# Kernel tuning notes

Measured on AMD Instinct MI355X. Metric: run time of the kernel, lower is better.

## Reference

```python
import jax, jax.numpy as jnp
import numpy as np
from jax.scipy.linalg import expm

B, S, D = 8, 2048, 1024          # batch, seq, input_dim
C, CD = 16, 64                   # num_concepts, concept_dim
L = C * CD                       # latent_dim = 1024
ALPHA, BETA = 0.3, 1.0
LN_EPS = 1e-5                    # torch nn.LayerNorm default


def layer_norm(x, g, b):
    m = jnp.mean(x, axis=-1, keepdims=True)
    v = jnp.mean(jnp.square(x - m), axis=-1, keepdims=True)
    return (x - m) * jax.lax.rsqrt(v + LN_EPS) * g + b


def setup_inputs() -> dict:
    key = jax.random.key(0)
    ks = jax.random.split(key, 8)
    sc = 0.02
    return {
        "x": jax.random.normal(ks[0], (B, S, D), jnp.float32),
        # encoder: Linear(D, 2L) + LayerNorm(2L)
        "enc_w": jax.random.normal(ks[1], (2 * L, D), jnp.float32) * sc,
        "enc_b": jnp.zeros((2 * L,), jnp.float32),
        "enc_g": jnp.ones((2 * L,), jnp.float32),
        "enc_bt": jnp.zeros((2 * L,), jnp.float32),
        # DAG weights [C, C] (torch inits zeros; use small random for non-trivial math)
        "dag_w": jax.random.normal(ks[2], (C, C), jnp.float32) * 0.1,
        # per-concept transforms: Linear(CD,CD) -> LN(CD) -> ReLU -> Linear(CD,CD), stacked over C
        "cw1": jax.random.normal(ks[3], (C, CD, CD), jnp.float32) * sc,
        "cb1": jnp.zeros((C, CD), jnp.float32),
        "cg": jnp.ones((C, CD), jnp.float32),
        "cbt": jnp.zeros((C, CD), jnp.float32),
        "cw2": jax.random.normal(ks[4], (C, CD, CD), jnp.float32) * sc,
        "cb2": jnp.zeros((C, CD), jnp.float32),
        # decoder: Linear(L,L) -> LN(L) -> ReLU -> Linear(L,D)
        "dec_w1": jax.random.normal(ks[5], (L, L), jnp.float32) * sc,
        "dec_b1": jnp.zeros((L,), jnp.float32),
        "dec_g": jnp.ones((L,), jnp.float32),
        "dec_bt": jnp.zeros((L,), jnp.float32),
        "dec_w2": jax.random.normal(ks[6], (D, L), jnp.float32) * sc,
        "dec_b2": jnp.zeros((D,), jnp.float32),
    }


def reference(x, enc_w, enc_b, enc_g, enc_bt, dag_w, cw1, cb1, cg, cbt, cw2, cb2,
              dec_w1, dec_b1, dec_g, dec_bt, dec_w2, dec_b2):
    # ---- encode ----
    h = layer_norm(jnp.einsum('bsd,kd->bsk', x, enc_w) + enc_b, enc_g, enc_bt)  # [B,S,2L]
    mu, logvar = jnp.split(h, 2, axis=-1)                                        # [B,S,L] each
    z = mu  # eval-mode reparameterize

    # ---- causal transform ----
    zc = z.reshape(B, S, C, CD)                                   # [B,S,C,CD]
    dag = jnp.tril(jax.nn.softplus(dag_w), k=-1)                  # [C,C]
    z_causal = zc + jnp.einsum('ij,bsjd->bsid', dag, zc)          # [B,S,C,CD]

    # per-concept Linear -> LN -> ReLU -> Linear, batched over concept axis
    t = jnp.einsum('bsce,cde->bscd', z_causal, cw1) + cb1         # [B,S,C,CD]
    t = layer_norm(t, cg, cbt)
    t = jax.nn.relu(t)
    t = jnp.einsum('bsce,cde->bscd', t, cw2) + cb2
    z_t = t.reshape(B, S, L)

    # ---- decode ----
    d = layer_norm(jnp.einsum('bsl,kl->bsk', z_t, dec_w1) + dec_b1, dec_g, dec_bt)
    d = jax.nn.relu(d)
    x_recon = jnp.einsum('bsl,dl->bsd', d, dec_w2) + dec_b2        # [B,S,D]

    # ---- losses ----
    recon_loss = jnp.mean(jnp.square(x_recon - x))
    kl_loss = -0.5 * jnp.mean(1.0 + logvar - jnp.square(mu) - jnp.exp(logvar))
    dag_loss = jnp.sum(jnp.abs(dag)) + jnp.trace(expm(dag))
    total_loss = recon_loss + ALPHA * kl_loss + BETA * dag_loss
    return x_recon, total_loss, kl_loss, recon_loss, dag_loss
```

## Files before the change

### kernel.cpp

```cpp
#include <hip/hip_runtime.h>
#include <stdint.h>


#define NTOK   16384
#define DIM    1024
#define NC     16
#define CD     64
#define NOUT_ELEMS 16777216

typedef float f32x4 __attribute__((ext_vector_type(4)));
typedef __bf16 bf16x8 __attribute__((ext_vector_type(8)));
typedef unsigned short u16x4 __attribute__((ext_vector_type(4)));
typedef unsigned short u16x8 __attribute__((ext_vector_type(8)));

__device__ float g_scal[3];
__device__ float g_part[512];

__device__ __forceinline__ float b2f(uint16_t u) {
  union { uint32_t i; float f; } v; v.i = ((uint32_t)u) << 16; return v.f;
}
__device__ __forceinline__ uint16_t f2b(float f) {
  union { float f; uint32_t i; } v; v.f = f;
  uint32_t x = v.i;
  return (uint16_t)((x + 0x7fffu + ((x >> 16) & 1u)) >> 16);
}

__device__ __forceinline__ void gload_lds16(const uint16_t* g, uint16_t* l) {
  __builtin_amdgcn_global_load_lds(
      (const __attribute__((address_space(1))) void*)g,
      (__attribute__((address_space(3))) void*)l, 16, 0, 0);
}

__device__ __forceinline__ void cvt8(const float* s, uint16_t* d) {
  const f32x4 a = *(const f32x4*)s;
  const f32x4 b = *(const f32x4*)(s + 4);
  u16x8 o;
  o[0]=f2b(a[0]); o[1]=f2b(a[1]); o[2]=f2b(a[2]); o[3]=f2b(a[3]);
  o[4]=f2b(b[0]); o[5]=f2b(b[1]); o[6]=f2b(b[2]); o[7]=f2b(b[3]);
  *(u16x8*)d = o;
}

__global__ __launch_bounds__(256) void cvt_x_kernel(
    const float* __restrict__ src, uint16_t* __restrict__ dst)
{
  const int i = blockIdx.x * 256 + threadIdx.x;
  cvt8(src + (size_t)i * 8, dst + (size_t)i * 8);
}

__global__ __launch_bounds__(256) void cvt_weights_kernel(
    const float* __restrict__ ew, const float* __restrict__ d1,
    const float* __restrict__ d2, const float* __restrict__ c1,
    const float* __restrict__ c2, uint16_t* __restrict__ out)
{
  const int i = blockIdx.x * 256 + threadIdx.x;
  const float* src; uint16_t* dst; int off;
  if (i < 262144)      { src = ew; dst = out;           off = i; }
  else if (i < 393216) { src = d1; dst = out + 2097152; off = i - 262144; }
  else if (i < 524288) { src = d2; dst = out + 3145728; off = i - 393216; }
  else if (i < 532480) { src = c1; dst = out + 4194304; off = i - 524288; }
  else                 { src = c2; dst = out + 4259840; off = i - 532480; }
  cvt8(src + (size_t)off * 8, dst + (size_t)off * 8);
}

template<int BM, int BN, int WM, int WN, typename TC, bool SPLIT>
__global__ __launch_bounds__(256) void gemm_bt_kernel(
    const uint16_t* __restrict__ A, const uint16_t* __restrict__ Wm,
    const float* __restrict__ bias, TC* __restrict__ C0, TC* __restrict__ C1,
    int K, int lda, int ldw, int ldc,
    int csA, int csW, int csB, int csC)
{
  constexpr int BK = 64;
  static_assert(WM * WN == 4, "4 waves");
  constexpr int MI = BM / (WM * 16);
  constexpr int NI = BN / (WN * 16);
  constexpr int AI = (BM * BK * 2) / 4096;
  constexpr int WI = (BN * BK * 2) / 4096;
  static_assert((BM * BK * 2) % 4096 == 0 && (BN * BK * 2) % 4096 == 0, "");

  __shared__ __align__(16) uint16_t lds[BM * BK + BN * BK];
  uint16_t* As = lds;
  uint16_t* Ws = lds + BM * BK;

  const int cz = blockIdx.z;
  A    += (size_t)cz * csA;
  Wm   += (size_t)cz * csW;
  bias += cz * csB;

  const int tid  = threadIdx.x;
  const int wave = tid >> 6;
  const int lane = tid & 63;
  const int q    = lane >> 4;
  const int r16  = lane & 15;
  const int wm   = wave / WN;
  const int wn   = wave % WN;

  const int bm = blockIdx.x * BM;
  const int bn = blockIdx.y * BN;

  const int sr = tid >> 3;
  const int pc = tid & 7;

  f32x4 acc[MI][NI] = {};

  for (int k0 = 0; k0 < K; k0 += BK) {
#pragma unroll
    for (int i = 0; i < AI; ++i) {
      const int r = i * 32 + sr;
      const int c = pc ^ (r & 7);
      const uint16_t* g = A + (size_t)(bm + r) * lda + k0 + c * 8;
      gload_lds16(g, (uint16_t*)((char*)As + i * 4096 + wave * 1024));
    }
#pragma unroll
    for (int i = 0; i < WI; ++i) {
      const int r = i * 32 + sr;
      const int c = pc ^ (r & 7);
      const uint16_t* g = Wm + (size_t)(bn + r) * ldw + k0 + c * 8;
      gload_lds16(g, (uint16_t*)((char*)Ws + i * 4096 + wave * 1024));
    }
    __syncthreads();

#pragma unroll
    for (int ks = 0; ks < 2; ++ks) {
      bf16x8 af[MI], wf[NI];
#pragma unroll
      for (int mi = 0; mi < MI; ++mi) {
        const int row = wm * (MI * 16) + mi * 16 + r16;
        const int c   = (ks * 4 + q) ^ (row & 7);
        af[mi] = *(const bf16x8*)(As + row * BK + c * 8);
      }
#pragma unroll
      for (int ni = 0; ni < NI; ++ni) {
        const int col = wn * (NI * 16) + ni * 16 + r16;
        const int c   = (ks * 4 + q) ^ (col & 7);
        wf[ni] = *(const bf16x8*)(Ws + col * BK + c * 8);
      }
#pragma unroll
      for (int mi = 0; mi < MI; ++mi)
#pragma unroll
        for (int ni = 0; ni < NI; ++ni)
          acc[mi][ni] = __builtin_amdgcn_mfma_f32_16x16x32_bf16(
              af[mi], wf[ni], acc[mi][ni], 0, 0, 0);
    }
    __syncthreads();
  }

  TC* Cq = C0;
  int cb = bn;
  if constexpr (SPLIT) {
    if (bn >= 1024) { Cq = C1; cb = bn - 1024; }
  }
  Cq += (size_t)cz * csC;
#pragma unroll
  for (int ni = 0; ni < NI; ++ni) {
    const int loc = wn * (NI * 16) + ni * 16 + r16;
    const float bv = bias[bn + loc];
#pragma unroll
    for (int mi = 0; mi < MI; ++mi) {
      const int rbase = bm + wm * (MI * 16) + mi * 16 + q * 4;
#pragma unroll
      for (int r = 0; r < 4; ++r) {
        const float v = acc[mi][ni][r] + bv;
        if constexpr (sizeof(TC) == 2)
          Cq[(size_t)(rbase + r) * ldc + cb + loc] = f2b(v);
        else
          Cq[(size_t)(rbase + r) * ldc + cb + loc] = v;
      }
    }
  }
}

__global__ __launch_bounds__(256) void kl_causal_kernel(
    const uint16_t* __restrict__ lv, uint16_t* __restrict__ mu,
    const float* __restrict__ g, const float* __restrict__ b,
    const float* __restrict__ dag_w)
{
  __shared__ __align__(16) float zsh[1024];
  __shared__ float dg[256];
  __shared__ float red[8];
  __shared__ float red2[4];
  const int tid = threadIdx.x;
  const int tok = blockIdx.x;
  const int e0  = tid * 4;

  {
    const int di = tid >> 4, dj = tid & 15;
    dg[tid] = (dj < di) ? log1pf(expf(dag_w[tid])) : 0.f;
  }

  const uint16_t* lvp = lv + (size_t)tok * 1024;
  uint16_t*       mup = mu + (size_t)tok * 1024;

  const u16x4 m4 = *(const u16x4*)(mup + e0);
  const u16x4 l4 = *(const u16x4*)(lvp + e0);
  float xm[4], xl[4];
  float s1 = 0.f, s2 = 0.f;
#pragma unroll
  for (int k = 0; k < 4; ++k) {
    xm[k] = b2f(m4[k]);
    xl[k] = b2f(l4[k]);
    s1 += xm[k] + xl[k];
    s2 += xm[k] * xm[k] + xl[k] * xl[k];
  }
#pragma unroll
  for (int m = 1; m < 64; m <<= 1) {
    s1 += __shfl_xor(s1, m);
    s2 += __shfl_xor(s2, m);
  }
  const int wave = tid >> 6, lane = tid & 63;
  if (lane == 0) { red[wave] = s1; red[4 + wave] = s2; }
  __syncthreads();
  s1 = red[0] + red[1] + red[2] + red[3];
  s2 = red[4] + red[5] + red[6] + red[7];
  const float mean = s1 * (1.f / 2048.f);
  const float var  = s2 * (1.f / 2048.f) - mean * mean;
  const float rs   = rsqrtf(var + 1e-5f);

  const f32x4 g4m = *(const f32x4*)(g + e0);
  const f32x4 b4m = *(const f32x4*)(b + e0);
  const f32x4 g4l = *(const f32x4*)(g + 1024 + e0);
  const f32x4 b4l = *(const f32x4*)(b + 1024 + e0);
  float kl = 0.f;
  f32x4 z;
#pragma unroll
  for (int k = 0; k < 4; ++k) {
    z[k] = (xm[k] - mean) * rs * g4m[k] + b4m[k];
    const float y = (xl[k] - mean) * rs * g4l[k] + b4l[k];
    kl += 1.f + y - z[k] * z[k] - expf(y);
  }
  *(f32x4*)(zsh + e0) = z;
#pragma unroll
  for (int m = 1; m < 64; m <<= 1) kl += __shfl_xor(kl, m);
  if (lane == 0) red2[wave] = kl;
  __syncthreads();
  if (tid == 0)
    atomicAdd(&g_part[tok & 255], red2[0] + red2[1] + red2[2] + red2[3]);

  const int i  = e0 >> 6;
  const int d0 = e0 & 63;
  f32x4 s = *(const f32x4*)(zsh + e0);
  for (int j = 0; j < i; ++j) {
    const float w = dg[i * 16 + j];
    const f32x4 zj = *(const f32x4*)(zsh + j * 64 + d0);
    s[0] += w * zj[0]; s[1] += w * zj[1]; s[2] += w * zj[2]; s[3] += w * zj[3];
  }
  u16x4 o;
#pragma unroll
  for (int k = 0; k < 4; ++k) o[k] = f2b(s[k]);
  *(u16x4*)(mup + e0) = o;
}

__global__ __launch_bounds__(256) void ln_relu_kernel(
    uint16_t* __restrict__ data, const float* __restrict__ g,
    const float* __restrict__ b)
{
  const int tid = threadIdx.x;
  const int e0  = tid * 4;
  uint16_t* p = data + (size_t)blockIdx.x * 1024;

  const u16x4 v4 = *(const u16x4*)(p + e0);
  float x[4];
  float s1 = 0.f, s2 = 0.f;
#pragma unroll
  for (int k = 0; k < 4; ++k) {
    x[k] = b2f(v4[k]);
    s1 += x[k];
    s2 += x[k] * x[k];
  }
#pragma unroll
  for (int m = 1; m < 64; m <<= 1) {
    s1 += __shfl_xor(s1, m);
    s2 += __shfl_xor(s2, m);
  }
  __shared__ float red[8];
  const int wave = tid >> 6, lane = tid & 63;
  if (lane == 0) { red[wave] = s1; red[4 + wave] = s2; }
  __syncthreads();
  s1 = red[0] + red[1] + red[2] + red[3];
  s2 = red[4] + red[5] + red[6] + red[7];
  const float mean = s1 * (1.f / 1024.f);
  const float var  = s2 * (1.f / 1024.f) - mean * mean;
  const float rs   = rsqrtf(var + 1e-5f);

  const f32x4 g4 = *(const f32x4*)(g + e0);
  const f32x4 b4 = *(const f32x4*)(b + e0);
  u16x4 o;
#pragma unroll
  for (int k = 0; k < 4; ++k) {
    const float y = (x[k] - mean) * rs * g4[k] + b4[k];
    o[k] = f2b(fmaxf(y, 0.f));
  }
  *(u16x4*)(p + e0) = o;
}

__global__ __launch_bounds__(256) void ln_cd_kernel(
    uint16_t* __restrict__ t, const float* __restrict__ cg,
    const float* __restrict__ cbt)
{
  const int tid = threadIdx.x;
  const int sub = tid >> 4;
  const int le  = tid & 15;
  const int gidx = blockIdx.x * 16 + sub;
  const int c = gidx & 15;
  const size_t off = (size_t)gidx * 64 + le * 4;

  const u16x4 v4 = *(const u16x4*)(t + off);
  float x[4];
  float s1 = 0.f, s2 = 0.f;
#pragma unroll
  for (int k = 0; k < 4; ++k) {
    x[k] = b2f(v4[k]);
    s1 += x[k];
    s2 += x[k] * x[k];
  }
#pragma unroll
  for (int m = 1; m < 16; m <<= 1) {
    s1 += __shfl_xor(s1, m);
    s2 += __shfl_xor(s2, m);
  }
  const float mean = s1 * (1.f / 64.f);
  const float var  = s2 * (1.f / 64.f) - mean * mean;
  const float rs   = rsqrtf(var + 1e-5f);

  const f32x4 cg4  = *(const f32x4*)(cg + c * 64 + le * 4);
  const f32x4 cbt4 = *(const f32x4*)(cbt + c * 64 + le * 4);
  u16x4 o;
#pragma unroll
  for (int k = 0; k < 4; ++k) {
    const float y = (x[k] - mean) * rs * cg4[k] + cbt4[k];
    o[k] = f2b(fmaxf(y, 0.f));
  }
  *(u16x4*)(t + off) = o;
}

__global__ __launch_bounds__(256) void recon_kernel(
    const float* __restrict__ xr, const float* __restrict__ x, int n4)
{
  const f32x4* xr4 = (const f32x4*)xr;
  const f32x4* x4  = (const f32x4*)x;
  float s = 0.f;
  for (int i = blockIdx.x * 256 + threadIdx.x; i < n4; i += gridDim.x * 256) {
    const f32x4 d = xr4[i] - x4[i];
    s += d[0] * d[0] + d[1] * d[1] + d[2] * d[2] + d[3] * d[3];
  }
#pragma unroll
  for (int m = 1; m < 64; m <<= 1) s += __shfl_xor(s, m);
  __shared__ float red[4];
  const int wave = threadIdx.x >> 6, lane = threadIdx.x & 63;
  if (lane == 0) red[wave] = s;
  __syncthreads();
  if (threadIdx.x == 0)
    atomicAdd(&g_part[256 + (blockIdx.x & 255)], red[0] + red[1] + red[2] + red[3]);
}

__global__ __launch_bounds__(256) void dag_init_kernel(
    const float* __restrict__ dag_w)
{
  const int t = threadIdx.x;
  g_part[t] = 0.f;
  g_part[256 + t] = 0.f;
  const int i = t >> 4, j = t & 15;
  const float v = (j < i) ? log1pf(expf(dag_w[t])) : 0.f;
  float s = v;
#pragma unroll
  for (int m = 1; m < 64; m <<= 1) s += __shfl_xor(s, m);
  __shared__ float red[4];
  const int wave = t >> 6, lane = t & 63;
  if (lane == 0) red[wave] = s;
  __syncthreads();
  if (t == 0)
    g_scal[2] = red[0] + red[1] + red[2] + red[3] + 16.f;
}

__global__ __launch_bounds__(256) void finalize_kernel(float* __restrict__ out_tail)
{
  const int tid = threadIdx.x;
  float kl = g_part[tid];
  float rc = g_part[256 + tid];
#pragma unroll
  for (int m = 1; m < 64; m <<= 1) {
    kl += __shfl_xor(kl, m);
    rc += __shfl_xor(rc, m);
  }
  __shared__ float red[8];
  const int wave = tid >> 6, lane = tid & 63;
  if (lane == 0) { red[wave] = kl; red[4 + wave] = rc; }
  __syncthreads();
  if (tid == 0) {
    const float kls = red[0] + red[1] + red[2] + red[3];
    const float rcs = red[4] + red[5] + red[6] + red[7];
    const float kl_l   = -0.5f * kls * (1.f / (16384.f * 1024.f));
    const float recon  = rcs * (1.f / 16777216.f);
    const float dagl   = g_scal[2];
    out_tail[0] = recon + 0.3f * kl_l + 1.0f * dagl;
    out_tail[1] = kl_l;
    out_tail[2] = recon;
    out_tail[3] = dagl;
  }
}

extern "C" void kernel_launch(void* const* d_in, const int* in_sizes, int n_in,
                              void* d_out, int out_size, void* d_ws, size_t ws_size,
                              hipStream_t stream) {
  const float* x      = (const float*)d_in[0];
  const float* enc_w  = (const float*)d_in[1];
  const float* enc_b  = (const float*)d_in[2];
  const float* enc_g  = (const float*)d_in[3];
  const float* enc_bt = (const float*)d_in[4];
  const float* dag_w  = (const float*)d_in[5];
  const float* cw1    = (const float*)d_in[6];
  const float* cb1    = (const float*)d_in[7];
  const float* cg     = (const float*)d_in[8];
  const float* cbt    = (const float*)d_in[9];
  const float* cw2    = (const float*)d_in[10];
  const float* cb2    = (const float*)d_in[11];
  const float* dec_w1 = (const float*)d_in[12];
  const float* dec_b1 = (const float*)d_in[13];
  const float* dec_g  = (const float*)d_in[14];
  const float* dec_bt = (const float*)d_in[15];
  const float* dec_w2 = (const float*)d_in[16];
  const float* dec_b2 = (const float*)d_in[17];

  uint16_t* S    = (uint16_t*)d_ws;
  uint16_t* Wbf  = (uint16_t*)((char*)d_ws + (size_t)NTOK * DIM * 2);
  uint16_t* ewb  = Wbf;
  uint16_t* d1b  = Wbf + 2097152;
  uint16_t* d2b  = Wbf + 3145728;
  uint16_t* c1b  = Wbf + 4194304;
  uint16_t* c2b  = Wbf + 4259840;

  uint16_t* Obf  = (uint16_t*)d_out;
  uint16_t* xbf  = Obf + (size_t)NOUT_ELEMS;
  float*    O    = (float*)d_out;

  dag_init_kernel<<<1, 256, 0, stream>>>(dag_w);

  cvt_x_kernel<<<NOUT_ELEMS / 8 / 256, 256, 0, stream>>>(x, xbf);
  cvt_weights_kernel<<<2112, 256, 0, stream>>>(enc_w, dec_w1, dec_w2, cw1, cw2, Wbf);

  gemm_bt_kernel<128, 128, 2, 2, uint16_t, true>
      <<<dim3(128, 16, 1), 256, 0, stream>>>(
      xbf, ewb, enc_b, Obf, S, DIM, DIM, DIM, DIM, 0, 0, 0, 0);

  kl_causal_kernel<<<NTOK, 256, 0, stream>>>(S, Obf, enc_g, enc_bt, dag_w);

  gemm_bt_kernel<128, 64, 4, 1, uint16_t, false>
      <<<dim3(128, 1, 16), 256, 0, stream>>>(
      Obf, c1b, cb1, S, S, CD, DIM, CD, DIM, 64, 4096, 64, 64);

  ln_cd_kernel<<<NTOK * NC / 16, 256, 0, stream>>>(S, cg, cbt);

  gemm_bt_kernel<128, 64, 4, 1, uint16_t, false>
      <<<dim3(128, 1, 16), 256, 0, stream>>>(
      S, c2b, cb2, Obf, Obf, CD, DIM, CD, DIM, 64, 4096, 64, 64);

  gemm_bt_kernel<128, 128, 2, 2, uint16_t, false>
      <<<dim3(128, 8, 1), 256, 0, stream>>>(
      Obf, d1b, dec_b1, S, S, DIM, DIM, DIM, DIM, 0, 0, 0, 0);

  ln_relu_kernel<<<NTOK, 256, 0, stream>>>(S, dec_g, dec_bt);

  gemm_bt_kernel<128, 128, 2, 2, float, false>
      <<<dim3(128, 8, 1), 256, 0, stream>>>(
      S, d2b, dec_b2, O, O, DIM, DIM, DIM, DIM, 0, 0, 0, 0);

  recon_kernel<<<1024, 256, 0, stream>>>(O, x, NOUT_ELEMS / 4);

  finalize_kernel<<<1, 256, 0, stream>>>(O + (size_t)NOUT_ELEMS);
}
```

Baseline: 459.5 us.

## Fuse per-concept MLP into one kernel and fold recon loss into decoder GEMM

Replaces the two per-concept batched GEMMs and the separate concept LayerNorm kernel with a single kernel. It keeps a 128x64 token tile in LDS, applies Linear, LayerNorm, ReLU and the second Linear, then writes the result in place. It also computes the squared reconstruction error in the final decoder GEMM epilogue, which removes the separate recon pass over the output and x. This cuts several full-size intermediate round trips through global memory and two kernel launches. The cost is an extra read of x inside the GEMM epilogue and a reduction plus atomic per block.

```diff
diff --git a/kernel.cpp b/kernel.cpp
--- a/kernel.cpp
+++ b/kernel.cpp
@@ -62,12 +62,12 @@
   cvt8(src + (size_t)off * 8, dst + (size_t)off * 8);
 }
 
-template<int BM, int BN, int WM, int WN, typename TC, bool SPLIT>
+template<int BM, int BN, int WM, int WN, typename TC, bool SPLIT, bool RECON>
 __global__ __launch_bounds__(256) void gemm_bt_kernel(
     const uint16_t* __restrict__ A, const uint16_t* __restrict__ Wm,
     const float* __restrict__ bias, TC* __restrict__ C0, TC* __restrict__ C1,
-    int K, int lda, int ldw, int ldc,
-    int csA, int csW, int csB, int csC)
+    const float* __restrict__ Xref,
+    int K, int lda, int ldw, int ldc)
 {
   constexpr int BK = 64;
   static_assert(WM * WN == 4, "4 waves");
@@ -75,16 +75,10 @@
   constexpr int NI = BN / (WN * 16);
   constexpr int AI = (BM * BK * 2) / 4096;
   constexpr int WI = (BN * BK * 2) / 4096;
-  static_assert((BM * BK * 2) % 4096 == 0 && (BN * BK * 2) % 4096 == 0, "");
 
   __shared__ __align__(16) uint16_t lds[BM * BK + BN * BK];
   uint16_t* As = lds;
   uint16_t* Ws = lds + BM * BK;
-
-  const int cz = blockIdx.z;
-  A    += (size_t)cz * csA;
-  Wm   += (size_t)cz * csW;
-  bias += cz * csB;
 
   const int tid  = threadIdx.x;
   const int wave = tid >> 6;
@@ -149,7 +143,7 @@
   if constexpr (SPLIT) {
     if (bn >= 1024) { Cq = C1; cb = bn - 1024; }
   }
-  Cq += (size_t)cz * csC;
+  float rsum = 0.f;
 #pragma unroll
   for (int ni = 0; ni < NI; ++ni) {
     const int loc = wn * (NI * 16) + ni * 16 + r16;
@@ -164,9 +158,158 @@
           Cq[(size_t)(rbase + r) * ldc + cb + loc] = f2b(v);
         else
           Cq[(size_t)(rbase + r) * ldc + cb + loc] = v;
-      }
-    }
-  }
+        if constexpr (RECON) {
+          const float dd = v - Xref[(size_t)(rbase + r) * ldc + cb + loc];
+          rsum += dd * dd;
+        }
+      }
+    }
+  }
+  if constexpr (RECON) {
+#pragma unroll
+    for (int m = 1; m < 64; m <<= 1) rsum += __shfl_xor(rsum, m);
+    __shared__ float redR[4];
+    if (lane == 0) redR[wave] = rsum;
+    __syncthreads();
+    if (tid == 0)
+      atomicAdd(&g_part[256 + ((blockIdx.x * 8 + blockIdx.y) & 255)],
+                redR[0] + redR[1] + redR[2] + redR[3]);
+  }
+}
+
+__global__ __launch_bounds__(256) void concept_fused_kernel(
+    uint16_t* __restrict__ z, const uint16_t* __restrict__ c1b,
+    const uint16_t* __restrict__ c2b, const float* __restrict__ cb1,
+    const float* __restrict__ cg, const float* __restrict__ cbt,
+    const float* __restrict__ cb2)
+{
+  __shared__ __align__(16) uint16_t Az[128 * 64];
+  __shared__ __align__(16) uint16_t W1s[64 * 64];
+  __shared__ __align__(16) uint16_t W2s[64 * 64];
+
+  const int tid  = threadIdx.x;
+  const int wave = tid >> 6;
+  const int lane = tid & 63;
+  const int q    = lane >> 4;
+  const int r16  = lane & 15;
+  const int c    = blockIdx.y;
+  const int m0   = blockIdx.x * 128;
+
+  const int lr = tid >> 3;
+  const int pc = tid & 7;
+
+#pragma unroll
+  for (int i = 0; i < 4; ++i) {
+    const int r = i * 32 + lr;
+    const int gc = pc ^ (r & 7);
+    gload_lds16(z + (size_t)(m0 + r) * DIM + c * 64 + gc * 8,
+                (uint16_t*)((char*)Az + i * 4096 + wave * 1024));
+  }
+#pragma unroll
+  for (int i = 0; i < 2; ++i) {
+    const int r = i * 32 + lr;
+    const int gc = pc ^ (r & 7);
+    gload_lds16(c1b + (size_t)c * 4096 + r * 64 + gc * 8,
+                (uint16_t*)((char*)W1s + i * 4096 + wave * 1024));
+    gload_lds16(c2b + (size_t)c * 4096 + r * 64 + gc * 8,
+                (uint16_t*)((char*)W2s + i * 4096 + wave * 1024));
+  }
+  __syncthreads();
+
+  f32x4 acc[2][4] = {};
+#pragma unroll
+  for (int ks = 0; ks < 2; ++ks) {
+    bf16x8 af[2], wf[4];
+#pragma unroll
+    for (int mi = 0; mi < 2; ++mi) {
+      const int row = wave * 32 + mi * 16 + r16;
+      af[mi] = *(const bf16x8*)(Az + row * 64 + ((ks * 4 + q) ^ (row & 7)) * 8);
+    }
+#pragma unroll
+    for (int ni = 0; ni < 4; ++ni) {
+      const int d = ni * 16 + r16;
+      wf[ni] = *(const bf16x8*)(W1s + d * 64 + ((ks * 4 + q) ^ (d & 7)) * 8);
+    }
+#pragma unroll
+    for (int mi = 0; mi < 2; ++mi)
+#pragma unroll
+      for (int ni = 0; ni < 4; ++ni)
+        acc[mi][ni] = __builtin_amdgcn_mfma_f32_16x16x32_bf16(
+            af[mi], wf[ni], acc[mi][ni], 0, 0, 0);
+  }
+
+  float b1v[4], cgv[4], cbv[4], b2v[4];
+#pragma unroll
+  for (int ni = 0; ni < 4; ++ni) {
+    const int cn = ni * 16 + r16;
+    b1v[ni] = cb1[c * 64 + cn];
+    cgv[ni] = cg[c * 64 + cn];
+    cbv[ni] = cbt[c * 64 + cn];
+    b2v[ni] = cb2[c * 64 + cn];
+  }
+#pragma unroll
+  for (int mi = 0; mi < 2; ++mi) {
+#pragma unroll
+    for (int r = 0; r < 4; ++r) {
+      float s1 = 0.f, s2 = 0.f;
+#pragma unroll
+      for (int ni = 0; ni < 4; ++ni) {
+        const float v = acc[mi][ni][r] + b1v[ni];
+        acc[mi][ni][r] = v;
+        s1 += v; s2 += v * v;
+      }
+#pragma unroll
+      for (int m = 1; m < 16; m <<= 1) {
+        s1 += __shfl_xor(s1, m);
+        s2 += __shfl_xor(s2, m);
+      }
+      const float mean = s1 * (1.f / 64.f);
+      const float var  = s2 * (1.f / 64.f) - mean * mean;
+      const float rs   = rsqrtf(var + 1e-5f);
+      const int row = wave * 32 + mi * 16 + q * 4 + r;
+#pragma unroll
+      for (int ni = 0; ni < 4; ++ni) {
+        const float y = fmaxf((acc[mi][ni][r] - mean) * rs * cgv[ni] + cbv[ni], 0.f);
+        const int cn = ni * 16 + r16;
+        Az[row * 64 + (((cn >> 3) ^ (row & 7)) * 8) + (cn & 7)] = f2b(y);
+      }
+    }
+  }
+  __syncthreads();
+
+  f32x4 acc2[2][4] = {};
+#pragma unroll
+  for (int ks = 0; ks < 2; ++ks) {
+    bf16x8 af[2], wf[4];
+#pragma unroll
+    for (int mi = 0; mi < 2; ++mi) {
+      const int row = wave * 32 + mi * 16 + r16;
+      af[mi] = *(const bf16x8*)(Az + row * 64 + ((ks * 4 + q) ^ (row & 7)) * 8);
+    }
+#pragma unroll
+    for (int ni = 0; ni < 4; ++ni) {
+      const int d = ni * 16 + r16;
+      wf[ni] = *(const bf16x8*)(W2s + d * 64 + ((ks * 4 + q) ^ (d & 7)) * 8);
+    }
+#pragma unroll
+    for (int mi = 0; mi < 2; ++mi)
+#pragma unroll
+      for (int ni = 0; ni < 4; ++ni)
+        acc2[mi][ni] = __builtin_amdgcn_mfma_f32_16x16x32_bf16(
+            af[mi], wf[ni], acc2[mi][ni], 0, 0, 0);
+  }
+
+#pragma unroll
+  for (int mi = 0; mi < 2; ++mi)
+#pragma unroll
+    for (int ni = 0; ni < 4; ++ni) {
+      const int cn = ni * 16 + r16;
+#pragma unroll
+      for (int r = 0; r < 4; ++r) {
+        const int row = wave * 32 + mi * 16 + q * 4 + r;
+        z[(size_t)(m0 + row) * DIM + c * 64 + cn] = f2b(acc2[mi][ni][r] + b2v[ni]);
+      }
+    }
 }
 
 __global__ __launch_bounds__(256) void kl_causal_kernel(
@@ -290,66 +433,6 @@
     o[k] = f2b(fmaxf(y, 0.f));
   }
   *(u16x4*)(p + e0) = o;
-}
-
-__global__ __launch_bounds__(256) void ln_cd_kernel(
-    uint16_t* __restrict__ t, const float* __restrict__ cg,
-    const float* __restrict__ cbt)
-{
-  const int tid = threadIdx.x;
-  const int sub = tid >> 4;
-  const int le  = tid & 15;
-  const int gidx = blockIdx.x * 16 + sub;
-  const int c = gidx & 15;
-  const size_t off = (size_t)gidx * 64 + le * 4;
-
-  const u16x4 v4 = *(const u16x4*)(t + off);
-  float x[4];
-  float s1 = 0.f, s2 = 0.f;
-#pragma unroll
-  for (int k = 0; k < 4; ++k) {
-    x[k] = b2f(v4[k]);
-    s1 += x[k];
-    s2 += x[k] * x[k];
-  }
-#pragma unroll
-  for (int m = 1; m < 16; m <<= 1) {
-    s1 += __shfl_xor(s1, m);
-    s2 += __shfl_xor(s2, m);
-  }
-  const float mean = s1 * (1.f / 64.f);
-  const float var  = s2 * (1.f / 64.f) - mean * mean;
-  const float rs   = rsqrtf(var + 1e-5f);
-
-  const f32x4 cg4  = *(const f32x4*)(cg + c * 64 + le * 4);
-  const f32x4 cbt4 = *(const f32x4*)(cbt + c * 64 + le * 4);
-  u16x4 o;
-#pragma unroll
-  for (int k = 0; k < 4; ++k) {
-    const float y = (x[k] - mean) * rs * cg4[k] + cbt4[k];
-    o[k] = f2b(fmaxf(y, 0.f));
-  }
-  *(u16x4*)(t + off) = o;
-}
-
-__global__ __launch_bounds__(256) void recon_kernel(
-    const float* __restrict__ xr, const float* __restrict__ x, int n4)
-{
-  const f32x4* xr4 = (const f32x4*)xr;
-  const f32x4* x4  = (const f32x4*)x;
-  float s = 0.f;
-  for (int i = blockIdx.x * 256 + threadIdx.x; i < n4; i += gridDim.x * 256) {
-    const f32x4 d = xr4[i] - x4[i];
-    s += d[0] * d[0] + d[1] * d[1] + d[2] * d[2] + d[3] * d[3];
-  }
-#pragma unroll
-  for (int m = 1; m < 64; m <<= 1) s += __shfl_xor(s, m);
-  __shared__ float red[4];
-  const int wave = threadIdx.x >> 6, lane = threadIdx.x & 63;
-  if (lane == 0) red[wave] = s;
-  __syncthreads();
-  if (threadIdx.x == 0)
-    atomicAdd(&g_part[256 + (blockIdx.x & 255)], red[0] + red[1] + red[2] + red[3]);
 }
 
 __global__ __launch_bounds__(256) void dag_init_kernel(
@@ -437,33 +520,24 @@
   cvt_x_kernel<<<NOUT_ELEMS / 8 / 256, 256, 0, stream>>>(x, xbf);
   cvt_weights_kernel<<<2112, 256, 0, stream>>>(enc_w, dec_w1, dec_w2, cw1, cw2, Wbf);
 
-  gemm_bt_kernel<128, 128, 2, 2, uint16_t, true>
+  gemm_bt_kernel<128, 128, 2, 2, uint16_t, true, false>
       <<<dim3(128, 16, 1), 256, 0, stream>>>(
-      xbf, ewb, enc_b, Obf, S, DIM, DIM, DIM, DIM, 0, 0, 0, 0);
+      xbf, ewb, enc_b, Obf, S, nullptr, DIM, DIM, DIM, DIM);
 
   kl_causal_kernel<<<NTOK, 256, 0, stream>>>(S, Obf, enc_g, enc_bt, dag_w);
 
-  gemm_bt_kernel<128, 64, 4, 1, uint16_t, false>
-      <<<dim3(128, 1, 16), 256, 0, stream>>>(
-      Obf, c1b, cb1, S, S, CD, DIM, CD, DIM, 64, 4096, 64, 64);
-
-  ln_cd_kernel<<<NTOK * NC / 16, 256, 0, stream>>>(S, cg, cbt);
-
-  gemm_bt_kernel<128, 64, 4, 1, uint16_t, false>
-      <<<dim3(128, 1, 16), 256, 0, stream>>>(
-      S, c2b, cb2, Obf, Obf, CD, DIM, CD, DIM, 64, 4096, 64, 64);
-
-  gemm_bt_kernel<128, 128, 2, 2, uint16_t, false>
+  concept_fused_kernel<<<dim3(128, 16, 1), 256, 0, stream>>>(
+      Obf, c1b, c2b, cb1, cg, cbt, cb2);
+
+  gemm_bt_kernel<128, 128, 2, 2, uint16_t, false, false>
       <<<dim3(128, 8, 1), 256, 0, stream>>>(
-      Obf, d1b, dec_b1, S, S, DIM, DIM, DIM, DIM, 0, 0, 0, 0);
+      Obf, d1b, dec_b1, S, S, nullptr, DIM, DIM, DIM, DIM);
 
   ln_relu_kernel<<<NTOK, 256, 0, stream>>>(S, dec_g, dec_bt);
 
-  gemm_bt_kernel<128, 128, 2, 2, float, false>
+  gemm_bt_kernel<128, 128, 2, 2, float, false, true>
       <<<dim3(128, 8, 1), 256, 0, stream>>>(
-      S, d2b, dec_b2, O, O, DIM, DIM, DIM, DIM, 0, 0, 0, 0);
-
-  recon_kernel<<<1024, 256, 0, stream>>>(O, x, NOUT_ELEMS / 4);
+      S, d2b, dec_b2, O, O, x, DIM, DIM, DIM, DIM);
 
   finalize_kernel<<<1, 256, 0, stream>>>(O + (size_t)NOUT_ELEMS);
 }
```

After: 424.2 us. -7.7%, faster.
